# Kernel tuning notes

Measured on AMD Instinct MI355X. Metric: run time of the kernel, lower is better.

## Reference

```python
import jax, jax.numpy as jnp
import numpy as np

EPS = 1e-8
NUM_HEADS = 8
SCALE = 25.0
SIM_THRESH = 0.75
BLOCK = 10  # per-frame proposal group size used by the zeroing mask


def _l2norm(x):
    return x / (jnp.linalg.norm(x, axis=-1, keepdims=True) + EPS)


def setup_inputs() -> dict:
    key = jax.random.key(0)
    ks = jax.random.split(key, 7)
    B, N, C = 1, 2000, 256
    H = NUM_HEADS
    x_cls = jax.random.normal(ks[0], (B, N, C), dtype=jnp.float32)
    x_reg = jax.random.normal(ks[1], (B, N, C), dtype=jnp.float32)
    cls_score = jax.random.uniform(ks[2], (N,), dtype=jnp.float32)
    fg_score = jax.random.uniform(ks[3], (N,), dtype=jnp.float32)
    coord_attn = jax.random.uniform(ks[4], (B, H, N, N), dtype=jnp.float32)
    W_qkv_cls = jax.random.normal(ks[5], (3 * C, C), dtype=jnp.float32) * 0.02
    W_qkv_reg = jax.random.normal(ks[6], (3 * C, C), dtype=jnp.float32) * 0.02
    return {"x_cls": x_cls, "x_reg": x_reg, "cls_score": cls_score,
            "fg_score": fg_score, "coord_attn": coord_attn,
            "W_qkv_cls": W_qkv_cls, "W_qkv_reg": W_qkv_reg}


def reference(x_cls, x_reg, cls_score, fg_score, coord_attn, W_qkv_cls, W_qkv_reg):
    B, N, C = x_cls.shape
    H = NUM_HEADS
    D = C // H

    def qkv(x, W):
        t = (x @ W.T).reshape(B, N, 3, H, D).transpose(2, 0, 3, 1, 4)  # [3,B,H,N,D]
        return t[0], t[1], t[2]

    q_cls, k_cls, v_cls = qkv(x_cls, W_qkv_cls)
    q_reg, k_reg, v_reg = qkv(x_reg, W_qkv_reg)

    q_cls, k_cls = _l2norm(q_cls), _l2norm(k_cls)
    q_reg, k_reg = _l2norm(q_reg), _l2norm(k_reg)
    v_cls_normed = _l2norm(v_cls)

    cs = cls_score.reshape(1, 1, 1, N)  # broadcast over [B,H,N,N]
    fs = fg_score.reshape(1, 1, 1, N)

    attn_cls_raw = jnp.einsum('bhnd,bhmd->bhnm', v_cls_normed, v_cls_normed)

    attn_cls = jax.nn.softmax(jnp.einsum('bhnd,bhmd->bhnm', q_cls, k_cls) * SCALE * cs, axis=-1)
    attn_reg = jax.nn.softmax(jnp.einsum('bhnd,bhmd->bhnm', q_reg, k_reg) * SCALE * fs, axis=-1)

    attn = (attn_reg + attn_cls) * 0.5 * coord_attn
    attn = jax.lax.stop_gradient(attn)  # original detaches before masking

    # block-diagonal zeroing: row j zeros cols [j//10*10, j//10*10+9), keep diagonal
    rows = jnp.arange(N)[:, None]
    cols = jnp.arange(N)[None, :]
    block_start = (rows // BLOCK) * BLOCK
    zero_mask = (cols >= block_start) & (cols < block_start + (BLOCK - 1)) & (cols != rows)
    attn = jnp.where(zero_mask, 0.0, attn)

    x = jnp.einsum('bhnm,bhmd->bhnd', attn, v_cls).transpose(0, 2, 1, 3).reshape(B, N, C)
    x_ori = v_cls.transpose(0, 2, 1, 3).reshape(B, N, C)
    x_cat = jnp.concatenate([x, x_ori], axis=-1)  # [B,N,2C]

    # ave=True branch
    sim_raw = jnp.sum(attn_cls_raw, axis=1)[0] / H          # [N,N]
    sim_mask = (sim_raw > SIM_THRESH).astype(x_cls.dtype)
    sim_attn = jnp.sum(attn, axis=1)[0] / H                 # [N,N]
    sim_round2 = jax.nn.softmax(sim_attn, axis=-1)
    sim_round2 = sim_mask * sim_round2 / (jnp.sum(sim_mask * sim_round2, axis=-1, keepdims=True) + EPS)
    return x_cat, sim_round2
```

## Files before the change

### kernel.cpp

```cpp
#include <hip/hip_runtime.h>
#include <math.h>

typedef _Float16 half8 __attribute__((ext_vector_type(8)));
typedef _Float16 half4 __attribute__((ext_vector_type(4)));
typedef _Float16 half2v __attribute__((ext_vector_type(2)));
typedef float f32x4 __attribute__((ext_vector_type(4)));

constexpr int N = 2000;
constexpr int NP = 2048;
constexpr int H = 8;
constexpr int D = 32;
constexpr float SCL = 25.0f;
constexpr float L2E = 1.4426950408889634f;
constexpr float FM2 = 25.0f * L2E;

#define MFMA16(a,b,c)  __builtin_amdgcn_mfma_f32_16x16x32_f16((a),(b),(c),0,0,0)
#define MFMA16K(a,b,c) __builtin_amdgcn_mfma_f32_16x16x16f16((a),(b),(c),0,0,0)

__device__ __forceinline__ float fexp2(float x) { return __builtin_amdgcn_exp2f(x); }


__global__ __launch_bounds__(256) void wconv_kernel(
    const float* __restrict__ Wc, const float* __restrict__ Wr,
    _Float16* __restrict__ Wch, _Float16* __restrict__ Wrh)
{
    const int i = blockIdx.x * 256 + threadIdx.x;
    Wch[i] = (_Float16)Wc[i];
    Wrh[i] = (_Float16)Wr[i];
}

__global__ __launch_bounds__(256) void qkv_kernel(
    const float* __restrict__ xc, const float* __restrict__ xr,
    const _Float16* __restrict__ Wch, const _Float16* __restrict__ Wrh,
    _Float16* __restrict__ Qch, _Float16* __restrict__ Kch,
    _Float16* __restrict__ Qrh, _Float16* __restrict__ Krh,
    _Float16* __restrict__ Vnh, _Float16* __restrict__ Vth,
    float* __restrict__ out)
{
    constexpr int XS = 264;
    __shared__ _Float16 xs[16 * XS];
    const int t = threadIdx.x;
    const int n0 = blockIdx.x * 16;
    const int by = blockIdx.y;
    const int which = (by < 3) ? by : (by - 3);
    const bool isCls = by < 3;
    const float* x = isCls ? xc : xr;
    const _Float16* Wh = isCls ? Wch : Wrh;

    #pragma unroll
    for (int it = 0; it < 4; ++it) {
        const int f = t + it * 256;
        const int row = f >> 6, c4 = f & 63;
        const float4 v = *(const float4*)(x + (size_t)(n0 + row) * 256 + c4 * 4);
        half4 hv; hv[0]=(_Float16)v.x; hv[1]=(_Float16)v.y; hv[2]=(_Float16)v.z; hv[3]=(_Float16)v.w;
        *(half4*)&xs[row * XS + c4 * 4] = hv;
    }
    __syncthreads();

    const int w = t >> 6, l = t & 63;
    const int lr = l & 15, lg = l >> 4;
    const int obase = which * 256 + w * 64;
    f32x4 acc[4] = {{0,0,0,0},{0,0,0,0},{0,0,0,0},{0,0,0,0}};
    for (int k0 = 0; k0 < 256; k0 += 32) {
        const half8 aX = *(const half8*)&xs[lr * XS + k0 + lg * 8];
        #pragma unroll
        for (int s = 0; s < 4; ++s) {
            const half8 bW = *(const half8*)(Wh + (size_t)(obase + s * 16 + lr) * 256 + k0 + lg * 8);
            acc[s] = MFMA16(aX, bW, acc[s]);
        }
    }
    #pragma unroll
    for (int p = 0; p < 2; ++p) {
        const int h = 2 * w + p;
        float ss[4];
        #pragma unroll
        for (int j = 0; j < 4; ++j) {
            float v = acc[2*p][j]*acc[2*p][j] + acc[2*p+1][j]*acc[2*p+1][j];
            #pragma unroll
            for (int off = 1; off < 16; off <<= 1) v += __shfl_xor(v, off);
            ss[j] = sqrtf(v) + 1e-8f;
        }
        if (which < 2) {
            _Float16* Qd = isCls ? (which == 0 ? Qch : Kch) : (which == 0 ? Qrh : Krh);
            #pragma unroll
            for (int sh = 0; sh < 2; ++sh)
                #pragma unroll
                for (int j = 0; j < 4; ++j)
                    Qd[((size_t)h*NP + n0 + lg*4 + j)*D + sh*16 + lr] = (_Float16)(acc[2*p+sh][j] / ss[j]);
        } else {
            #pragma unroll
            for (int sh = 0; sh < 2; ++sh) {
                const int d = sh * 16 + lr;
                half4 tv;
                #pragma unroll
                for (int j = 0; j < 4; ++j) {
                    const float raw = acc[2*p+sh][j];
                    Vnh[((size_t)h*NP + n0 + lg*4 + j)*D + d] = (_Float16)(raw / ss[j]);
                    out[(size_t)(n0 + lg*4 + j)*512 + 256 + h*D + d] = raw;
                    tv[j] = (_Float16)raw;
                }
                *(half4*)(Vth + ((size_t)h*D + d)*NP + n0 + lg*4) = tv;
            }
        }
    }
}

__global__ __launch_bounds__(512) void stats_kernel(
    const _Float16* __restrict__ Qch, const _Float16* __restrict__ Kch,
    const _Float16* __restrict__ Qrh, const _Float16* __restrict__ Krh,
    const float* __restrict__ clsScore, const float* __restrict__ fgScore,
    float* __restrict__ STi)
{
    __shared__ float Ssh[4][2][16];
    const int t = threadIdx.x;
    const int w = t >> 6, l = t & 63;
    const int nsub = w >> 1, mhalf = w & 1;
    const int n0 = blockIdx.x * 64 + nsub * 16;
    const int h = blockIdx.y, z = blockIdx.z;
    const _Float16* Q = z ? Qrh : Qch;
    const _Float16* K = z ? Krh : Kch;
    const float* score = z ? fgScore : clsScore;
    const int lr = l & 15, lg = l >> 4;
    const half8 aQ = *(const half8*)(Q + ((size_t)h*NP + n0 + lr)*D + lg*8);
    float S[4] = {0.f, 0.f, 0.f, 0.f};
    const int msBeg = mhalf ? 63 : 0;
    const int msEnd = mhalf ? 125 : 63;
    half8 bK = *(const half8*)(K + ((size_t)h*NP + msBeg*16 + lr)*D + lg*8);
    float sc = score[msBeg*16 + lr];
    for (int ms = msBeg; ms < msEnd; ++ms) {
        const half8 cur = bK;
        const float scc = sc;
        if (ms + 1 < msEnd) {
            bK = *(const half8*)(K + ((size_t)h*NP + (ms+1)*16 + lr)*D + lg*8);
            sc = score[(ms+1)*16 + lr];
        }
        f32x4 z4 = {0.f, 0.f, 0.f, 0.f};
        const f32x4 c = MFMA16(aQ, cur, z4);
        const float sm2 = scc * (SCL * L2E);
        #pragma unroll
        for (int j = 0; j < 4; ++j) S[j] += fexp2(fmaf(c[j], sm2, -FM2));
    }
    #pragma unroll
    for (int j = 0; j < 4; ++j) {
        #pragma unroll
        for (int off = 1; off < 16; off <<= 1) S[j] += __shfl_xor(S[j], off);
    }
    if (lr == 0) {
        #pragma unroll
        for (int j = 0; j < 4; ++j) Ssh[nsub][mhalf][lg*4 + j] = S[j];
    }
    __syncthreads();
    if (t < 64) {
        const int ns = t >> 4, rl = t & 15;
        STi[((size_t)z*H + h)*NP + blockIdx.x*64 + ns*16 + rl]
            = 1.f / (Ssh[ns][0][rl] + Ssh[ns][1][rl]);
    }
}

__global__ __launch_bounds__(256) void vvmask_kernel(
    const _Float16* __restrict__ Vnh, unsigned char* __restrict__ Mask)
{
    const int t = threadIdx.x;
    const int w = t >> 6, l = t & 63;
    const int n0 = blockIdx.y * 16;
    const int m00 = blockIdx.x * 256 + w * 64;
    const int lr = l & 15, lg = l >> 4;
    half8 aV[8];
    #pragma unroll
    for (int h = 0; h < 8; ++h)
        aV[h] = *(const half8*)(Vnh + ((size_t)(h*NP + n0 + lr))*D + lg*8);
    for (int s = 0; s < 4; ++s) {
        const int mb = m00 + s*16;
        f32x4 acc = {0.f, 0.f, 0.f, 0.f};
        #pragma unroll
        for (int h = 0; h < 8; ++h) {
            const half8 bV = *(const half8*)(Vnh + ((size_t)(h*NP + mb + lr))*D + lg*8);
            acc = MFMA16(aV[h], bV, acc);
        }
        const int m = mb + lr;
        if (m < N) {
            #pragma unroll
            for (int j = 0; j < 4; ++j) {
                const int n = n0 + lg*4 + j;
                Mask[(size_t)n*N + m] = (acc[j]*0.125f > 0.75f) ? (unsigned char)1 : (unsigned char)0;
            }
        }
    }
}

struct Stage {
    half8 aQc, aQr;
    half8 bKc[2], bKr[2];
    f32x4 co[2];
    float iC, iR;
};

__global__ __launch_bounds__(256) void attn_kernel(
    const _Float16* __restrict__ Qch, const _Float16* __restrict__ Kch,
    const _Float16* __restrict__ Qrh, const _Float16* __restrict__ Krh,
    const _Float16* __restrict__ Vth, const float* __restrict__ coord,
    const float* __restrict__ clsScore, const float* __restrict__ fgScore,
    const float* __restrict__ STi,
    _Float16* __restrict__ SIMH, _Float16* __restrict__ XPH)
{
    __shared__ _Float16 pvred[2][4][2][16][18];

    const int t = threadIdx.x;
    const int w = t >> 6, l = t & 63;
    const int lr = l & 15, lg = l >> 4;
    const int mc = blockIdx.x;
    const int m0 = mc * 128;
    const int n0 = blockIdx.y * 16;
    const int n  = n0 + lr;
    const int bs = (n / 10) * 10;
    const int cb = w * 32;

    int mb[2]; bool ok[2];
    #pragma unroll
    for (int s = 0; s < 2; ++s) { mb[s] = m0 + cb + s*16; ok[s] = mb[s] < N; }

    f32x4 sc4[2], sf4[2];
    #pragma unroll
    for (int s = 0; s < 2; ++s) {
        sc4[s] = ok[s] ? (SCL*L2E) * *(const f32x4*)(clsScore + mb[s] + lg*4) : (f32x4){0,0,0,0};
        sf4[s] = ok[s] ? (SCL*L2E) * *(const f32x4*)(fgScore  + mb[s] + lg*4) : (f32x4){0,0,0,0};
    }
    float simacc[2][4] = {{0,0,0,0},{0,0,0,0}};

    auto loadStage = [&](int h, Stage& st) {
        st.iC = STi[(size_t)h*NP + n];
        st.iR = STi[((size_t)(H + h))*NP + n];
        st.aQc = *(const half8*)(Qch + ((size_t)h*NP + n)*D + lg*8);
        st.aQr = *(const half8*)(Qrh + ((size_t)h*NP + n)*D + lg*8);
        #pragma unroll
        for (int s = 0; s < 2; ++s) {
            if (ok[s]) {
                st.bKc[s] = *(const half8*)(Kch + ((size_t)h*NP + mb[s] + lr)*D + lg*8);
                st.bKr[s] = *(const half8*)(Krh + ((size_t)h*NP + mb[s] + lr)*D + lg*8);
                st.co[s]  = *(const f32x4*)(coord + ((size_t)h*N + n)*N + mb[s] + lg*4);
            }
        }
    };

    auto computeHead = [&](int h, const Stage& st) {
        half4 bV0[2], bV1[2];
        #pragma unroll
        for (int s = 0; s < 2; ++s) if (ok[s]) {
            bV0[s] = *(const half4*)(Vth + ((size_t)(h*D + lr))*NP + mb[s] + lg*4);
            bV1[s] = *(const half4*)(Vth + ((size_t)(h*D + 16 + lr))*NP + mb[s] + lg*4);
        }
        f32x4 pvA[2][2] = {{{0,0,0,0},{0,0,0,0}},{{0,0,0,0},{0,0,0,0}}};
        #pragma unroll
        for (int s = 0; s < 2; ++s) {
            if (!ok[s]) continue;
            f32x4 z4 = {0.f,0.f,0.f,0.f};
            const f32x4 cc = MFMA16(st.bKc[s], st.aQc, z4);
            const f32x4 cr = MFMA16(st.bKr[s], st.aQr, z4);
            half4 af;
            #pragma unroll
            for (int j = 0; j < 4; ++j) {
                const int m = mb[s] + lg*4 + j;
                float a = (fexp2(fmaf(cc[j], sc4[s][j], -FM2)) * st.iC
                         + fexp2(fmaf(cr[j], sf4[s][j], -FM2)) * st.iR) * 0.5f * st.co[s][j];
                if (m >= bs && m < bs+9 && m != n) a = 0.f;
                simacc[s][j] += a;
                af[j] = (_Float16)a;
            }
            pvA[s][0] = MFMA16K(af, bV0[s], pvA[s][0]);
            pvA[s][1] = MFMA16K(af, bV1[s], pvA[s][1]);
        }
        const f32x4 pv0 = pvA[0][0] + pvA[1][0];
        const f32x4 pv1 = pvA[0][1] + pvA[1][1];
        const int buf = h & 1;
        half4 h0, h1;
        #pragma unroll
        for (int j = 0; j < 4; ++j) { h0[j] = (_Float16)pv0[j]; h1[j] = (_Float16)pv1[j]; }
        *(half4*)&pvred[buf][w][0][lr][lg*4] = h0;
        *(half4*)&pvred[buf][w][1][lr][lg*4] = h1;
        asm volatile("s_waitcnt lgkmcnt(0)" ::: "memory");
        __builtin_amdgcn_s_barrier();
        const size_t xbase = ((size_t)(mc*H + h)*N + n0)*D;
        {
            const int e0 = 2*t;
            const int d = e0 & 15, db = (e0 >> 4) & 1, q = e0 >> 5;
            const float s0 = (float)pvred[buf][0][db][d][q]   + (float)pvred[buf][1][db][d][q]
                           + (float)pvred[buf][2][db][d][q]   + (float)pvred[buf][3][db][d][q];
            const float s1 = (float)pvred[buf][0][db][d+1][q] + (float)pvred[buf][1][db][d+1][q]
                           + (float)pvred[buf][2][db][d+1][q] + (float)pvred[buf][3][db][d+1][q];
            half2v o; o[0] = (_Float16)s0; o[1] = (_Float16)s1;
            *(half2v*)(XPH + xbase + e0) = o;
        }
    };

    Stage A, B;
    loadStage(0, A);
    #pragma unroll
    for (int hp = 0; hp < H; hp += 2) {
        loadStage(hp + 1, B);
        computeHead(hp, A);
        if (hp + 2 < H) loadStage(hp + 2, A);
        computeHead(hp + 1, B);
    }

    #pragma unroll
    for (int s = 0; s < 2; ++s) {
        if (!ok[s]) continue;
        half4 v;
        #pragma unroll
        for (int j = 0; j < 4; ++j) v[j] = (_Float16)(simacc[s][j] * 0.125f);
        *(half4*)(SIMH + (size_t)n*N + mb[s] + lg*4) = v;
    }
}

__global__ __launch_bounds__(256) void reduce_kernel(
    const _Float16* __restrict__ XPH, float* __restrict__ out)
{
    const int n = blockIdx.x, t = threadIdx.x;
    const int h = t >> 5, d = t & 31;
    float acc = 0.f;
    #pragma unroll
    for (int mcI = 0; mcI < 16; ++mcI)
        acc += (float)XPH[(((size_t)mcI*H + h)*N + n)*D + d];
    out[(size_t)n*512 + t] = acc;
}

__global__ __launch_bounds__(256) void simfinal_kernel(
    const _Float16* __restrict__ SIMH, const unsigned char* __restrict__ Mask,
    float* __restrict__ out)
{
    __shared__ float redA[4], redB[4];
    const int n = blockIdx.x, t = threadIdx.x;
    const _Float16* row = SIMH + (size_t)n * N;
    const unsigned char* mrow = Mask + (size_t)n * N;
    const bool act = t < 250;
    float f[8];
    unsigned int mk0 = 0, mk1 = 0;
    float mx = -1e30f;
    if (act) {
        const half8 v8 = *(const half8*)(row + t*8);
        const uint2 mm = *(const uint2*)(mrow + t*8);
        mk0 = mm.x; mk1 = mm.y;
        #pragma unroll
        for (int k = 0; k < 8; ++k) { f[k] = (float)v8[k]; mx = fmaxf(mx, f[k]); }
    }
    #pragma unroll
    for (int off = 1; off < 64; off <<= 1) mx = fmaxf(mx, __shfl_xor(mx, off));
    const int wv = t >> 6;
    if ((t & 63) == 0) redA[wv] = mx;
    __syncthreads();
    const float M = fmaxf(fmaxf(redA[0], redA[1]), fmaxf(redA[2], redA[3]));
    float e[8];
    float sA = 0.f, sM = 0.f;
    if (act) {
        #pragma unroll
        for (int k = 0; k < 8; ++k) {
            e[k] = fexp2((f[k] - M) * L2E);
            sA += e[k];
            const unsigned int mkb = ((k < 4 ? mk0 : mk1) >> (8*(k & 3))) & 0xffu;
            if (mkb) sM += e[k]; else e[k] = 0.f;
        }
    }
    #pragma unroll
    for (int off = 1; off < 64; off <<= 1) { sA += __shfl_xor(sA, off); sM += __shfl_xor(sM, off); }
    __syncthreads();
    if ((t & 63) == 0) { redA[wv] = sA; redB[wv] = sM; }
    __syncthreads();
    const float SA = redA[0] + redA[1] + redA[2] + redA[3];
    const float SMK = redB[0] + redB[1] + redB[2] + redB[3];
    const float inv = 1.f / (SMK + 1e-8f * SA);
    if (act) {
        float* orow = out + 1024000 + (size_t)n*N + t*8;
        *(float4*)(orow)     = make_float4(e[0]*inv, e[1]*inv, e[2]*inv, e[3]*inv);
        *(float4*)(orow + 4) = make_float4(e[4]*inv, e[5]*inv, e[6]*inv, e[7]*inv);
    }
}

extern "C" void kernel_launch(void* const* d_in, const int* in_sizes, int n_in,
                              void* d_out, int out_size, void* d_ws, size_t ws_size,
                              hipStream_t stream) {
    const float* x_cls     = (const float*)d_in[0];
    const float* x_reg     = (const float*)d_in[1];
    const float* cls_score = (const float*)d_in[2];
    const float* fg_score  = (const float*)d_in[3];
    const float* coord     = (const float*)d_in[4];
    const float* Wc        = (const float*)d_in[5];
    const float* Wr        = (const float*)d_in[6];

    char* base = (char*)d_ws;
    float* STi      = (float*)base;
    _Float16* SIMH  = (_Float16*)(base + 131072);
    _Float16* XPH   = (_Float16*)(base + 8131072);
    _Float16* Qch   = (_Float16*)(base + 24515072);
    _Float16* Kch   = Qch + 524288;
    _Float16* Qrh   = Qch + 2*524288;
    _Float16* Krh   = Qch + 3*524288;
    _Float16* Vnh   = Qch + 4*524288;
    _Float16* Vth   = Qch + 5*524288;
    _Float16* Wch   = (_Float16*)(base + 30806528);
    _Float16* Wrh   = (_Float16*)(base + 31199744);
    unsigned char* Mask = (unsigned char*)(base + 31592960);
    float* out = (float*)d_out;

    wconv_kernel<<<768, 256, 0, stream>>>(Wc, Wr, Wch, Wrh);
    qkv_kernel<<<dim3(125, 5), 256, 0, stream>>>(x_cls, x_reg, Wch, Wrh,
                                                 Qch, Kch, Qrh, Krh, Vnh, Vth, out);
    stats_kernel<<<dim3(32, 8, 2), 512, 0, stream>>>(Qch, Kch, Qrh, Krh, cls_score, fg_score, STi);
    vvmask_kernel<<<dim3(8, 125), 256, 0, stream>>>(Vnh, Mask);
    attn_kernel<<<dim3(16, 125), 256, 0, stream>>>(Qch, Kch, Qrh, Krh, Vth, coord,
                                                   cls_score, fg_score, STi, SIMH, XPH);
    reduce_kernel<<<2000, 256, 0, stream>>>(XPH, out);
    simfinal_kernel<<<2000, 256, 0, stream>>>(SIMH, Mask, out);
}
```

Baseline: 142.2 us.

## Fold score scaling into K and softmax normalizer into log-bias; restructure attn work split

Pre-multiplies K by score*25*log2e in the QKV kernel so the logits come straight out of the MFMA. The per-row softmax normalizer and the 0.5 factor are folded into an additive log2 bias, which turns each probability into a single exp2 of (logit+bias). The attention kernel is reorganized so that each wave owns two heads and walks all 128 columns, with only a final LDS reduction for the similarity sum. This removes the per-head barrier and shared-memory PV reduction. The ragged tail is handled by a separate template instantiation, and the 1/8 head average moves into simfinal's exponent, trading fp16 accumulation precision for fewer multiplies.

```diff
diff --git a/kernel.cpp b/kernel.cpp
--- a/kernel.cpp
+++ b/kernel.cpp
@@ -32,6 +32,7 @@
 __global__ __launch_bounds__(256) void qkv_kernel(
     const float* __restrict__ xc, const float* __restrict__ xr,
     const _Float16* __restrict__ Wch, const _Float16* __restrict__ Wrh,
+    const float* __restrict__ clsScore, const float* __restrict__ fgScore,
     _Float16* __restrict__ Qch, _Float16* __restrict__ Kch,
     _Float16* __restrict__ Qrh, _Float16* __restrict__ Krh,
     _Float16* __restrict__ Vnh, _Float16* __restrict__ Vth,
@@ -69,6 +70,11 @@
             acc[s] = MFMA16(aX, bW, acc[s]);
         }
     }
+    f32x4 kscale = {1.f,1.f,1.f,1.f};
+    if (which == 1) {
+        const float* sp = isCls ? clsScore : fgScore;
+        kscale = (SCL * L2E) * *(const f32x4*)(sp + n0 + lg*4);
+    }
     #pragma unroll
     for (int p = 0; p < 2; ++p) {
         const int h = 2 * w + p;
@@ -86,7 +92,8 @@
             for (int sh = 0; sh < 2; ++sh)
                 #pragma unroll
                 for (int j = 0; j < 4; ++j)
-                    Qd[((size_t)h*NP + n0 + lg*4 + j)*D + sh*16 + lr] = (_Float16)(acc[2*p+sh][j] / ss[j]);
+                    Qd[((size_t)h*NP + n0 + lg*4 + j)*D + sh*16 + lr]
+                        = (_Float16)(acc[2*p+sh][j] / ss[j] * kscale[j]);
         } else {
             #pragma unroll
             for (int sh = 0; sh < 2; ++sh) {
@@ -108,8 +115,7 @@
 __global__ __launch_bounds__(512) void stats_kernel(
     const _Float16* __restrict__ Qch, const _Float16* __restrict__ Kch,
     const _Float16* __restrict__ Qrh, const _Float16* __restrict__ Krh,
-    const float* __restrict__ clsScore, const float* __restrict__ fgScore,
-    float* __restrict__ STi)
+    float* __restrict__ BIAS)
 {
     __shared__ float Ssh[4][2][16];
     const int t = threadIdx.x;
@@ -119,26 +125,20 @@
     const int h = blockIdx.y, z = blockIdx.z;
     const _Float16* Q = z ? Qrh : Qch;
     const _Float16* K = z ? Krh : Kch;
-    const float* score = z ? fgScore : clsScore;
     const int lr = l & 15, lg = l >> 4;
     const half8 aQ = *(const half8*)(Q + ((size_t)h*NP + n0 + lr)*D + lg*8);
     float S[4] = {0.f, 0.f, 0.f, 0.f};
     const int msBeg = mhalf ? 63 : 0;
     const int msEnd = mhalf ? 125 : 63;
     half8 bK = *(const half8*)(K + ((size_t)h*NP + msBeg*16 + lr)*D + lg*8);
-    float sc = score[msBeg*16 + lr];
     for (int ms = msBeg; ms < msEnd; ++ms) {
         const half8 cur = bK;
-        const float scc = sc;
-        if (ms + 1 < msEnd) {
+        if (ms + 1 < msEnd)
             bK = *(const half8*)(K + ((size_t)h*NP + (ms+1)*16 + lr)*D + lg*8);
-            sc = score[(ms+1)*16 + lr];
-        }
         f32x4 z4 = {0.f, 0.f, 0.f, 0.f};
         const f32x4 c = MFMA16(aQ, cur, z4);
-        const float sm2 = scc * (SCL * L2E);
-        #pragma unroll
-        for (int j = 0; j < 4; ++j) S[j] += fexp2(fmaf(c[j], sm2, -FM2));
+        #pragma unroll
+        for (int j = 0; j < 4; ++j) S[j] += fexp2(c[j] - FM2);
     }
     #pragma unroll
     for (int j = 0; j < 4; ++j) {
@@ -152,8 +152,8 @@
     __syncthreads();
     if (t < 64) {
         const int ns = t >> 4, rl = t & 15;
-        STi[((size_t)z*H + h)*NP + blockIdx.x*64 + ns*16 + rl]
-            = 1.f / (Ssh[ns][0][rl] + Ssh[ns][1][rl]);
+        BIAS[((size_t)z*H + h)*NP + blockIdx.x*64 + ns*16 + rl]
+            = -__log2f(Ssh[ns][0][rl] + Ssh[ns][1][rl]) - FM2 - 1.0f;
     }
 }
 
@@ -188,127 +188,110 @@
     }
 }
 
-struct Stage {
-    half8 aQc, aQr;
-    half8 bKc[2], bKr[2];
-    f32x4 co[2];
-    float iC, iR;
-};
-
-__global__ __launch_bounds__(256) void attn_kernel(
-    const _Float16* __restrict__ Qch, const _Float16* __restrict__ Kch,
-    const _Float16* __restrict__ Qrh, const _Float16* __restrict__ Krh,
+template<int SMAX>
+__global__ __launch_bounds__(256, 4) void attn_kernel(
+    const _Float16* __restrict__ Kch, const _Float16* __restrict__ Krh,
+    const _Float16* __restrict__ Qch, const _Float16* __restrict__ Qrh,
     const _Float16* __restrict__ Vth, const float* __restrict__ coord,
-    const float* __restrict__ clsScore, const float* __restrict__ fgScore,
-    const float* __restrict__ STi,
-    _Float16* __restrict__ SIMH, _Float16* __restrict__ XPH)
-{
-    __shared__ _Float16 pvred[2][4][2][16][18];
+    const float* __restrict__ BIAS,
+    _Float16* __restrict__ SIMH, _Float16* __restrict__ XPH, int mcBase)
+{
+    __shared__ _Float16 simred[4][16][136];
 
     const int t = threadIdx.x;
     const int w = t >> 6, l = t & 63;
     const int lr = l & 15, lg = l >> 4;
-    const int mc = blockIdx.x;
+    const int mc = mcBase + blockIdx.x;
     const int m0 = mc * 128;
     const int n0 = blockIdx.y * 16;
-    const int n  = n0 + lr;
+    const int n = n0 + lr;
     const int bs = (n / 10) * 10;
-    const int cb = w * 32;
-
-    int mb[2]; bool ok[2];
-    #pragma unroll
-    for (int s = 0; s < 2; ++s) { mb[s] = m0 + cb + s*16; ok[s] = mb[s] < N; }
-
-    f32x4 sc4[2], sf4[2];
-    #pragma unroll
-    for (int s = 0; s < 2; ++s) {
-        sc4[s] = ok[s] ? (SCL*L2E) * *(const f32x4*)(clsScore + mb[s] + lg*4) : (f32x4){0,0,0,0};
-        sf4[s] = ok[s] ? (SCL*L2E) * *(const f32x4*)(fgScore  + mb[s] + lg*4) : (f32x4){0,0,0,0};
-    }
-    float simacc[2][4] = {{0,0,0,0},{0,0,0,0}};
-
-    auto loadStage = [&](int h, Stage& st) {
-        st.iC = STi[(size_t)h*NP + n];
-        st.iR = STi[((size_t)(H + h))*NP + n];
-        st.aQc = *(const half8*)(Qch + ((size_t)h*NP + n)*D + lg*8);
-        st.aQr = *(const half8*)(Qrh + ((size_t)h*NP + n)*D + lg*8);
-        #pragma unroll
-        for (int s = 0; s < 2; ++s) {
-            if (ok[s]) {
-                st.bKc[s] = *(const half8*)(Kch + ((size_t)h*NP + mb[s] + lr)*D + lg*8);
-                st.bKr[s] = *(const half8*)(Krh + ((size_t)h*NP + mb[s] + lr)*D + lg*8);
-                st.co[s]  = *(const f32x4*)(coord + ((size_t)h*N + n)*N + mb[s] + lg*4);
+    const int h0 = 2 * w;
+
+    unsigned kill = 0u;
+    #pragma unroll
+    for (int s = 0; s < SMAX; ++s)
+        #pragma unroll
+        for (int j = 0; j < 4; ++j) {
+            const int m = m0 + s*16 + lg*4 + j;
+            if (m >= bs && m < bs + 9 && m != n) kill |= (1u << (s*4 + j));
+        }
+
+    half8 aQc[2], aQr[2]; float bC[2], bR[2];
+    #pragma unroll
+    for (int p = 0; p < 2; ++p) {
+        const int h = h0 + p;
+        aQc[p] = *(const half8*)(Qch + ((size_t)h*NP + n)*D + lg*8);
+        aQr[p] = *(const half8*)(Qrh + ((size_t)h*NP + n)*D + lg*8);
+        bC[p] = BIAS[(size_t)h*NP + n];
+        bR[p] = BIAS[(size_t)(H + h)*NP + n];
+    }
+
+    half2v sacc[SMAX][2];
+    #pragma unroll
+    for (int s = 0; s < SMAX; ++s)
+        #pragma unroll
+        for (int k = 0; k < 2; ++k) { sacc[s][k][0] = (_Float16)0.f; sacc[s][k][1] = (_Float16)0.f; }
+
+    half8 kc[2], kr[2]; half4 v0[2], v1[2]; f32x4 co[2];
+    auto LOAD = [&](int it) {
+        const int p = it / SMAX, s = it % SMAX, b = it & 1;
+        const int h = h0 + p;
+        const size_t kb = ((size_t)h*NP + m0 + s*16 + lr)*D + lg*8;
+        kc[b] = *(const half8*)(Kch + kb);
+        kr[b] = *(const half8*)(Krh + kb);
+        v0[b] = *(const half4*)(Vth + ((size_t)(h*D + lr))*NP + m0 + s*16 + lg*4);
+        v1[b] = *(const half4*)(Vth + ((size_t)(h*D + 16 + lr))*NP + m0 + s*16 + lg*4);
+        co[b] = *(const f32x4*)(coord + ((size_t)h*N + n)*N + m0 + s*16 + lg*4);
+    };
+
+    f32x4 pv0 = {0,0,0,0}, pv1 = {0,0,0,0};
+    LOAD(0);
+    #pragma unroll
+    for (int it = 0; it < 2*SMAX; ++it) {
+        const int p = it / SMAX, s = it % SMAX, b = it & 1;
+        if (it + 1 < 2*SMAX) LOAD(it + 1);
+        f32x4 z4 = {0.f,0.f,0.f,0.f};
+        const f32x4 cc = MFMA16(kc[b], aQc[p], z4);
+        const f32x4 cr = MFMA16(kr[b], aQr[p], z4);
+        half4 af;
+        #pragma unroll
+        for (int j = 0; j < 4; ++j) {
+            float a = (fexp2(cc[j] + bC[p]) + fexp2(cr[j] + bR[p])) * co[b][j];
+            if ((kill >> (s*4 + j)) & 1u) a = 0.f;
+            af[j] = (_Float16)a;
+        }
+        sacc[s][0] += (half2v){af[0], af[1]};
+        sacc[s][1] += (half2v){af[2], af[3]};
+        pv0 = MFMA16K(af, v0[b], pv0);
+        pv1 = MFMA16K(af, v1[b], pv1);
+        if (s == SMAX - 1) {
+            const int h = h0 + p;
+            _Float16* xp = XPH + (((size_t)(mc*H + h)*N + n0 + lg*4))*D + lr;
+            #pragma unroll
+            for (int j = 0; j < 4; ++j) {
+                xp[j*D]      = (_Float16)pv0[j];
+                xp[j*D + 16] = (_Float16)pv1[j];
             }
-        }
-    };
-
-    auto computeHead = [&](int h, const Stage& st) {
-        half4 bV0[2], bV1[2];
-        #pragma unroll
-        for (int s = 0; s < 2; ++s) if (ok[s]) {
-            bV0[s] = *(const half4*)(Vth + ((size_t)(h*D + lr))*NP + mb[s] + lg*4);
-            bV1[s] = *(const half4*)(Vth + ((size_t)(h*D + 16 + lr))*NP + mb[s] + lg*4);
-        }
-        f32x4 pvA[2][2] = {{{0,0,0,0},{0,0,0,0}},{{0,0,0,0},{0,0,0,0}}};
-        #pragma unroll
-        for (int s = 0; s < 2; ++s) {
-            if (!ok[s]) continue;
-            f32x4 z4 = {0.f,0.f,0.f,0.f};
-            const f32x4 cc = MFMA16(st.bKc[s], st.aQc, z4);
-            const f32x4 cr = MFMA16(st.bKr[s], st.aQr, z4);
-            half4 af;
-            #pragma unroll
-            for (int j = 0; j < 4; ++j) {
-                const int m = mb[s] + lg*4 + j;
-                float a = (fexp2(fmaf(cc[j], sc4[s][j], -FM2)) * st.iC
-                         + fexp2(fmaf(cr[j], sf4[s][j], -FM2)) * st.iR) * 0.5f * st.co[s][j];
-                if (m >= bs && m < bs+9 && m != n) a = 0.f;
-                simacc[s][j] += a;
-                af[j] = (_Float16)a;
-            }
-            pvA[s][0] = MFMA16K(af, bV0[s], pvA[s][0]);
-            pvA[s][1] = MFMA16K(af, bV1[s], pvA[s][1]);
-        }
-        const f32x4 pv0 = pvA[0][0] + pvA[1][0];
-        const f32x4 pv1 = pvA[0][1] + pvA[1][1];
-        const int buf = h & 1;
-        half4 h0, h1;
-        #pragma unroll
-        for (int j = 0; j < 4; ++j) { h0[j] = (_Float16)pv0[j]; h1[j] = (_Float16)pv1[j]; }
-        *(half4*)&pvred[buf][w][0][lr][lg*4] = h0;
-        *(half4*)&pvred[buf][w][1][lr][lg*4] = h1;
-        asm volatile("s_waitcnt lgkmcnt(0)" ::: "memory");
-        __builtin_amdgcn_s_barrier();
-        const size_t xbase = ((size_t)(mc*H + h)*N + n0)*D;
-        {
-            const int e0 = 2*t;
-            const int d = e0 & 15, db = (e0 >> 4) & 1, q = e0 >> 5;
-            const float s0 = (float)pvred[buf][0][db][d][q]   + (float)pvred[buf][1][db][d][q]
-                           + (float)pvred[buf][2][db][d][q]   + (float)pvred[buf][3][db][d][q];
-            const float s1 = (float)pvred[buf][0][db][d+1][q] + (float)pvred[buf][1][db][d+1][q]
-                           + (float)pvred[buf][2][db][d+1][q] + (float)pvred[buf][3][db][d+1][q];
-            half2v o; o[0] = (_Float16)s0; o[1] = (_Float16)s1;
-            *(half2v*)(XPH + xbase + e0) = o;
-        }
-    };
-
-    Stage A, B;
-    loadStage(0, A);
-    #pragma unroll
-    for (int hp = 0; hp < H; hp += 2) {
-        loadStage(hp + 1, B);
-        computeHead(hp, A);
-        if (hp + 2 < H) loadStage(hp + 2, A);
-        computeHead(hp + 1, B);
-    }
-
-    #pragma unroll
-    for (int s = 0; s < 2; ++s) {
-        if (!ok[s]) continue;
-        half4 v;
-        #pragma unroll
-        for (int j = 0; j < 4; ++j) v[j] = (_Float16)(simacc[s][j] * 0.125f);
-        *(half4*)(SIMH + (size_t)n*N + mb[s] + lg*4) = v;
+            pv0 = (f32x4){0,0,0,0}; pv1 = (f32x4){0,0,0,0};
+        }
+    }
+
+    #pragma unroll
+    for (int s = 0; s < SMAX; ++s) {
+        half4 sv; sv[0]=sacc[s][0][0]; sv[1]=sacc[s][0][1]; sv[2]=sacc[s][1][0]; sv[3]=sacc[s][1][1];
+        *(half4*)&simred[w][lr][s*16 + lg*4] = sv;
+    }
+    __syncthreads();
+    constexpr int C8 = SMAX * 2;
+    for (int e = t; e < 16 * C8; e += 256) {
+        const int r = e / C8, c8 = e % C8;
+        const half8 s0 = *(const half8*)&simred[0][r][c8*8];
+        const half8 s1 = *(const half8*)&simred[1][r][c8*8];
+        const half8 s2 = *(const half8*)&simred[2][r][c8*8];
+        const half8 s3 = *(const half8*)&simred[3][r][c8*8];
+        const half8 sum = (s0 + s1) + (s2 + s3);
+        *(half8*)(SIMH + (size_t)(n0 + r)*N + m0 + c8*8) = sum;
     }
 }
 
@@ -354,7 +337,7 @@
     if (act) {
         #pragma unroll
         for (int k = 0; k < 8; ++k) {
-            e[k] = fexp2((f[k] - M) * L2E);
+            e[k] = fexp2((f[k] - M) * (L2E * 0.125f));
             sA += e[k];
             const unsigned int mkb = ((k < 4 ? mk0 : mk1) >> (8*(k & 3))) & 0xffu;
             if (mkb) sM += e[k]; else e[k] = 0.f;
@@ -387,7 +370,7 @@
     const float* Wr        = (const float*)d_in[6];
 
     char* base = (char*)d_ws;
-    float* STi      = (float*)base;
+    float* BIAS     = (float*)base;
     _Float16* SIMH  = (_Float16*)(base + 131072);
     _Float16* XPH   = (_Float16*)(base + 8131072);
     _Float16* Qch   = (_Float16*)(base + 24515072);
@@ -402,12 +385,14 @@
     float* out = (float*)d_out;
 
     wconv_kernel<<<768, 256, 0, stream>>>(Wc, Wr, Wch, Wrh);
-    qkv_kernel<<<dim3(125, 5), 256, 0, stream>>>(x_cls, x_reg, Wch, Wrh,
+    qkv_kernel<<<dim3(125, 5), 256, 0, stream>>>(x_cls, x_reg, Wch, Wrh, cls_score, fg_score,
                                                  Qch, Kch, Qrh, Krh, Vnh, Vth, out);
-    stats_kernel<<<dim3(32, 8, 2), 512, 0, stream>>>(Qch, Kch, Qrh, Krh, cls_score, fg_score, STi);
+    stats_kernel<<<dim3(32, 8, 2), 512, 0, stream>>>(Qch, Kch, Qrh, Krh, BIAS);
     vvmask_kernel<<<dim3(8, 125), 256, 0, stream>>>(Vnh, Mask);
-    attn_kernel<<<dim3(16, 125), 256, 0, stream>>>(Qch, Kch, Qrh, Krh, Vth, coord,
-                                                   cls_score, fg_score, STi, SIMH, XPH);
+    attn_kernel<8><<<dim3(15, 125), 256, 0, stream>>>(Kch, Krh, Qch, Qrh, Vth, coord,
+                                                      BIAS, SIMH, XPH, 0);
+    attn_kernel<5><<<dim3(1, 125), 256, 0, stream>>>(Kch, Krh, Qch, Qrh, Vth, coord,
+                                                     BIAS, SIMH, XPH, 15);
     reduce_kernel<<<2000, 256, 0, stream>>>(XPH, out);
     simfinal_kernel<<<2000, 256, 0, stream>>>(SIMH, Mask, out);
 }
```

Result: no change. 144.2 us (+1.5%).
